# Kernel tuning notes

Measured on AMD Instinct MI355X. Metric: run time of the kernel, lower is better.

## Reference

```python
import jax, jax.numpy as jnp
import numpy as np

# ---- constants hardcoded in the original source ----
N_RBF = 50            # number of RBF policy centers
n = 4                 # cartpole state dim [x, xdot, theta, thetadot]
H = 60                # rollout horizon (hardcoded inside get_future_reward)
DT = 0.05             # dt_outer
KAPPA = 1.0           # UT spread parameter
JITTER = 1e-6
PROC_NOISE = 1e-2     # per-step process noise variance
# dynamics_params = [polemass_length, gravity, length, masspole, total_mass]
PML, G, LEN, MP, MT = 0.05, 9.8, 0.5, 0.1, 1.1

_diag_idx = np.arange(n)
_lr, _lc = np.tril_indices(n, -1)


def _build_L(sp):
    # sp: (N_RBF, n + n(n-1)/2) -> lower-triangular Cholesky factors (N_RBF, n, n)
    L = jnp.zeros((N_RBF, n, n), sp.dtype)
    L = L.at[:, _diag_idx, _diag_idx].set(sp[:, :n])
    L = L.at[:, _lr, _lc].set(sp[:, n:])
    return L


def _policy(params, x):
    # RBF policy: u = sum_i w_i * exp(-(x-mu_i)^T L_i L_i^T (x-mu_i)), clipped to force limits
    w = params[:N_RBF]
    mu = params[N_RBF:N_RBF + n * N_RBF].reshape(n, N_RBF)
    L = _build_L(params[N_RBF + n * N_RBF:].reshape(N_RBF, n + (n * n - n) // 2))
    d = x[:, None] - mu                          # (n, N)
    Ld = jnp.einsum('Nkj,kN->Nj', L, d)          # L_i^T d_i  -> (N, n)
    phi = jnp.exp(-jnp.sum(Ld * Ld, axis=1))     # (N,)
    return jnp.clip(jnp.dot(w, phi), -10.0, 10.0)


def _dyn(x, u):
    # gym cartpole continuous dynamics; x: (4, P) columns of sigma points
    pos, vel, th, thd = x
    s, c = jnp.sin(th), jnp.cos(th)
    temp = (u + PML * thd ** 2 * s) / MT
    thacc = (G * s - c * temp) / (LEN * (4.0 / 3.0 - MP * c * c / MT))
    xacc = temp - PML * thacc * c / MT
    return jnp.stack([vel, xacc, thd, thacc])


def _ut_weights(dtype):
    w0 = KAPPA / (n + KAPPA)
    wi = 1.0 / (2.0 * (n + KAPPA))
    return jnp.concatenate([jnp.array([w0], dtype), jnp.full((2 * n,), wi, dtype)])


def _gen_sigma(mu, cov):
    # standard unscented-transform sigma points from (mu, cov)
    S = jnp.linalg.cholesky(cov + JITTER * jnp.eye(n, dtype=mu.dtype))
    root = jnp.sqrt(n + KAPPA) * S               # (n, n)
    pts = jnp.concatenate([mu[:, None], mu[:, None] + root, mu[:, None] - root], axis=1)  # (n, 2n+1)
    return pts, _ut_weights(mu.dtype)


def _reward(states, weights):
    # quadratic cost UT-mean evaluator
    pos, vel, th, thd = states
    cost = pos ** 2 + vel ** 2 + 10.0 * th ** 2 + thd ** 2
    return -jnp.dot(weights, cost)


def _rollout(params, x0):
    states, weights = _gen_sigma(x0, jnp.zeros((n, n), x0.dtype))  # initialize sigma points at x0

    def body(carry, _):
        states, weights = carry                       # (4, 9), (9,)
        mean = states @ weights                        # UT mean
        u = _policy(params, mean)
        # sigma_point_expand: propagate each point, expand with process-noise UT points
        next_means = states + DT * _dyn(states, u)     # (4, 9)
        cov = PROC_NOISE * DT * jnp.eye(n, dtype=x0.dtype)
        S = jnp.linalg.cholesky(cov + JITTER * jnp.eye(n, dtype=x0.dtype))
        root = jnp.sqrt(n + KAPPA) * S
        offsets = jnp.concatenate([jnp.zeros((n, 1), x0.dtype), root, -root], axis=1)  # (4, 9)
        exp_states = (next_means[:, :, None] + offsets[:, None, :]).reshape(n, -1)      # (4, 81)
        ut_w = _ut_weights(x0.dtype)
        exp_weights = (weights[:, None] * ut_w[None, :]).reshape(-1)                    # (81,)
        # sigma_point_compress: moment-match and regenerate 2n+1 points
        m = exp_states @ exp_weights
        d = exp_states - m[:, None]
        covc = (d * exp_weights) @ d.T
        states, weights = _gen_sigma(m, covc)
        return (states, weights), _reward(states, weights)

    _, rewards = jax.lax.scan(body, (states, weights), None, length=H)
    return jnp.sum(rewards)


def setup_inputs() -> dict:
    key = jax.random.key(0)
    num_params = N_RBF + n * N_RBF + N_RBF * (n + (n * n - n) // 2)  # 750
    param = jax.random.normal(key, (num_params,), jnp.float32) * 0.1
    return {"param": param}


def reference(param):
    x0 = jnp.array([0.0, 0.0, 0.1, 0.0], param.dtype)
    return _rollout(param, x0)
```

## Files before the change

### kernel.cpp

```cpp
#include <hip/hip_runtime.h>
#include <math.h>


template <int CTRL>
__device__ __forceinline__ float dpp_add_f(float v) {
    int s = __builtin_amdgcn_update_dpp(0, __float_as_int(v), CTRL, 0xF, 0xF, true);
    return v + __int_as_float(s);
}
__device__ __forceinline__ float row_sum_f(float v) {
    v = dpp_add_f<0xB1>(v);
    v = dpp_add_f<0x4E>(v);
    v = dpp_add_f<0x124>(v);
    v = dpp_add_f<0x128>(v);
    return v;
}
__device__ __forceinline__ float lane_f(float v, int lane) {
    return __int_as_float(__builtin_amdgcn_readlane(__float_as_int(v), lane));
}
__device__ __forceinline__ float wave_sum_f(float v) {
    v = row_sum_f(v);
    v = dpp_add_f<0x142>(v);
    v = dpp_add_f<0x143>(v);
    return lane_f(v, 63);
}

__global__ __launch_bounds__(64) void horizon_kernel(const float* __restrict__ p,
                                                     float* __restrict__ out) {
    const int l   = threadIdx.x;
    const int l15 = l & 15;
    const int row = l >> 4;

    const float SQL2E = 1.2011224087864498f;

    float w = 0.0f, mu0 = 0.0f, mu1 = 0.0f, mu2 = 0.0f, mu3 = 0.0f;
    float s0=0,s1=0,s2=0,s3=0,s4=0,s5=0,s6=0,s7=0,s8=0,s9=0;
    if (l < 50) {
        w   = p[l];
        mu0 = p[ 50 + l]; mu1 = p[100 + l]; mu2 = p[150 + l]; mu3 = p[200 + l];
        const float* q = p + 250 + 10 * l;
        s0 = q[0]*SQL2E; s1 = q[1]*SQL2E; s2 = q[2]*SQL2E; s3 = q[3]*SQL2E;
        s4 = q[4]*SQL2E; s5 = q[5]*SQL2E; s6 = q[6]*SQL2E; s7 = q[7]*SQL2E;
        s8 = q[8]*SQL2E; s9 = q[9]*SQL2E;
    }

    const float wlf  = (l15 == 0) ? 0.2f : ((l15 < 9) ? 0.1f : 0.0f);
    const float fw5  = 5.0f * wlf;
    const float osgn = (l15 >= 1 && l15 <= 4) ? 1.0f
                     : ((l15 >= 5 && l15 <= 8) ? -1.0f : 0.0f);
    const int   ocol = ((l15 >= 5 ? l15 - 5 : l15 - 1) & 3);

    double mm0 = 0.0, mm1 = 0.0, mm2 = 0.1, mm3 = 0.0;
    float mmf0 = 0.0f, mmf1 = 0.0f, mmf2 = 0.1f, mmf3 = 0.0f;
    float d0 = mmf0 - mu0, d1 = mmf1 - mu1, d2 = mmf2 - mu2, d3 = mmf3 - mu3;
    float frmf = (float)(0.1 * 0.15915494309189535);
    const float CI = 2.2360679774997896e-3f;
    float c00=CI, c10=0.f, c20=0.f, c30=0.f;
    float c11=CI, c21=0.f, c31=0.f;
    float c22=CI, c32=0.f;
    float c33=CI;
    double acc = 0.0;

    const float DIAG5 = 0.00251f;

    #pragma unroll 4
    for (int t = 0; t < 60; ++t) {
        float t0v = fmaf(s0, d0, fmaf(s4, d1, fmaf(s5, d2, s7 * d3)));
        float t1v = fmaf(s1, d1, fmaf(s6, d2, s8 * d3));
        float t2v = fmaf(s2, d2, s9 * d3);
        float t3v = s3 * d3;
        float qn = fmaf(t0v, t0v, fmaf(t1v, t1v, fmaf(t2v, t2v, t3v * t3v)));
        float val = wave_sum_f(w * __builtin_amdgcn_exp2f(-qn));
        float u = fminf(10.0f, fmaxf(-10.0f, val));

        float oo0 = osgn * ((ocol == 0) ? c00 : 0.0f);
        float oo1 = osgn * ((ocol == 0) ? c10 : ((ocol == 1) ? c11 : 0.0f));
        float oo2 = osgn * ((ocol == 0) ? c20 : ((ocol == 1) ? c21 :
                            ((ocol == 2) ? c22 : 0.0f)));
        float oo3 = osgn * ((ocol == 0) ? c30 : ((ocol == 1) ? c31 :
                            ((ocol == 2) ? c32 : c33)));

        float x1 = mmf1 + oo1;
        float x3 = mmf3 + oo3;

        float rv = __builtin_amdgcn_fractf(fmaf(oo2, 0.15915494309189535f, frmf));
        float sn = __builtin_amdgcn_sinf(rv);
        float cs = __builtin_amdgcn_cosf(rv);
        float temp  = fmaf(0.05f * (x3 * x3), sn, u) * 0.9090909090909091f;
        float csc   = cs * cs;
        float den   = fmaf(csc, -0.045454545454545456f, 0.6666666666666666f);
        float rden  = __builtin_amdgcn_rcpf(den);
        float thacc = fmaf(9.8f, sn, -(cs * temp)) * rden;
        float xacc  = fmaf(-0.045454545454545456f, thacc * cs, temp);

        float dl0 = fmaf(0.05f, x1,    oo0);
        float dl1 = fmaf(0.05f, xacc,  oo1);
        float dl2 = fmaf(0.05f, x3,    oo2);
        float dl3 = fmaf(0.05f, thacc, oo3);

        float rd0 = row_sum_f(wlf * dl0);
        float rd1 = row_sum_f(wlf * dl1);
        float rd2 = row_sum_f(wlf * dl2);
        float rd3 = row_sum_f(wlf * dl3);

        mm0 += (double)rd0; mm1 += (double)rd1;
        mm2 += (double)rd2; mm3 += (double)rd3;
        mmf0 = (float)mm0; mmf1 = (float)mm1;
        mmf2 = (float)mm2; mmf3 = (float)mm3;
        d0 = mmf0 - mu0; d1 = mmf1 - mu1; d2 = mmf2 - mu2; d3 = mmf3 - mu3;
        double rev = mm2 * 0.15915494309189535;
        frmf = (float)(rev - floor(rev));

        float v0 = dl0 - rd0, v1 = dl1 - rd1, v2 = dl2 - rd2, v3 = dl3 - rd3;
        float a1 = (row == 0) ? v0 : v3;
        float b1 = (row <= 1) ? v0 : ((row == 2) ? v1 : v3);
        float a2 = (row <= 1) ? v1 : v2;
        float b2 = (row == 0) ? v0 : ((row == 1) ? v1 : v2);
        float a3 = (row <= 1) ? v2 : v3;
        float P1 = row_sum_f(fw5 * a1 * b1);
        float P2 = row_sum_f(fw5 * a2 * b2);
        float P3 = row_sum_f(fw5 * a3 * b2);

        float A00 = lane_f(P1,  0) + DIAG5;
        float A30 = lane_f(P1, 16);
        float A31 = lane_f(P1, 32);
        float A33 = lane_f(P1, 48) + DIAG5;
        float A10 = lane_f(P2,  0);
        float A11 = lane_f(P2, 16) + DIAG5;
        float A22 = lane_f(P2, 32) + DIAG5;
        float A20 = lane_f(P3,  0);
        float A21 = lane_f(P3, 16);
        float A32 = lane_f(P3, 32);

        float rwm = fmaf(mmf0, mmf0, fmaf(mmf1, mmf1,
                    fmaf(10.0f * mmf2, mmf2, mmf3 * mmf3)));
        float rwa = A00 + A11 + 10.0f * A22 + A33;
        acc -= (double)fmaf(0.2f, rwa, rwm);

        float i0 = __builtin_amdgcn_rsqf(A00);
        c00 = A00 * i0;
        c10 = A10 * i0; c20 = A20 * i0; c30 = A30 * i0;
        float b11 = fmaf(-c10, c10, A11);
        float i1 = __builtin_amdgcn_rsqf(b11);
        c11 = b11 * i1;
        c21 = fmaf(-c20, c10, A21) * i1;
        c31 = fmaf(-c30, c10, A31) * i1;
        float b22 = fmaf(-c21, c21, fmaf(-c20, c20, A22));
        float i2 = __builtin_amdgcn_rsqf(b22);
        c22 = b22 * i2;
        c32 = fmaf(-c31, c21, fmaf(-c30, c20, A32)) * i2;
        float b33 = fmaf(-c32, c32, fmaf(-c31, c31, fmaf(-c30, c30, A33)));
        c33 = b33 * __builtin_amdgcn_rsqf(b33);
    }

    if (l == 0) out[0] = (float)acc;
}

extern "C" void kernel_launch(void* const* d_in, const int* in_sizes, int n_in,
                              void* d_out, int out_size, void* d_ws, size_t ws_size,
                              hipStream_t stream) {
    (void)in_sizes; (void)n_in; (void)out_size; (void)d_ws; (void)ws_size;
    const float* p = (const float*)d_in[0];
    float* out = (float*)d_out;
    hipLaunchKernelGGL(horizon_kernel, dim3(1), dim3(64), 0, stream, p, out);
}
```

Baseline: 73.29 us.

## Overlap policy evaluation with covariance update by splitting dynamics affine in control

Rewrites the per-step dynamics so each sigma point's update is affine in the control u (alpha + beta*u). The mean and covariance reductions that do not depend on u can then run before or alongside the RBF policy wave reduction, shortening the serial dependency chain per step. The mean accumulators and the reward accumulator move from double to float, with only the angle phase kept in double. Unroll is lowered from 4 to 2. This adds extra reductions for the beta terms and risks small precision drift from float accumulation.

```diff
diff --git a/kernel.cpp b/kernel.cpp
--- a/kernel.cpp
+++ b/kernel.cpp
@@ -14,23 +14,28 @@
     v = dpp_add_f<0x128>(v);
     return v;
 }
-__device__ __forceinline__ float lane_f(float v, int lane) {
+__device__ __forceinline__ float rl(float v, int lane) {
     return __int_as_float(__builtin_amdgcn_readlane(__float_as_int(v), lane));
 }
 __device__ __forceinline__ float wave_sum_f(float v) {
     v = row_sum_f(v);
     v = dpp_add_f<0x142>(v);
     v = dpp_add_f<0x143>(v);
-    return lane_f(v, 63);
+    return rl(v, 63);
 }
 
 __global__ __launch_bounds__(64) void horizon_kernel(const float* __restrict__ p,
                                                      float* __restrict__ out) {
     const int l   = threadIdx.x;
     const int l15 = l & 15;
-    const int row = l >> 4;
+    const bool r1 = (l >> 4) & 1, r2 = (l >> 4) & 2;
 
-    const float SQL2E = 1.2011224087864498f;
+    const float SQL2E  = 1.2011224087864498f;
+    const float INV_MT = 0.9090909090909091f;
+    const float KCS    = -0.045454545454545456f;
+    const double INV2PI_D = 0.15915494309189535;
+    const float  INV2PI_F = 0.15915494309189535f;
+    const float DIAG5  = 0.00251f;
 
     float w = 0.0f, mu0 = 0.0f, mu1 = 0.0f, mu2 = 0.0f, mu3 = 0.0f;
     float s0=0,s1=0,s2=0,s3=0,s4=0,s5=0,s6=0,s7=0,s8=0,s9=0;
@@ -49,29 +54,19 @@
                      : ((l15 >= 5 && l15 <= 8) ? -1.0f : 0.0f);
     const int   ocol = ((l15 >= 5 ? l15 - 5 : l15 - 1) & 3);
 
-    double mm0 = 0.0, mm1 = 0.0, mm2 = 0.1, mm3 = 0.0;
     float mmf0 = 0.0f, mmf1 = 0.0f, mmf2 = 0.1f, mmf3 = 0.0f;
-    float d0 = mmf0 - mu0, d1 = mmf1 - mu1, d2 = mmf2 - mu2, d3 = mmf3 - mu3;
-    float frmf = (float)(0.1 * 0.15915494309189535);
+    float d0 = -mu0, d1 = -mu1, d2 = 0.1f - mu2, d3 = -mu3;
+    double rev = 0.1 * INV2PI_D;
+    float frmf = (float)rev;
     const float CI = 2.2360679774997896e-3f;
     float c00=CI, c10=0.f, c20=0.f, c30=0.f;
     float c11=CI, c21=0.f, c31=0.f;
     float c22=CI, c32=0.f;
     float c33=CI;
-    double acc = 0.0;
+    float acc = 0.0f;
 
-    const float DIAG5 = 0.00251f;
-
-    #pragma unroll 4
+    #pragma unroll 2
     for (int t = 0; t < 60; ++t) {
-        float t0v = fmaf(s0, d0, fmaf(s4, d1, fmaf(s5, d2, s7 * d3)));
-        float t1v = fmaf(s1, d1, fmaf(s6, d2, s8 * d3));
-        float t2v = fmaf(s2, d2, s9 * d3);
-        float t3v = s3 * d3;
-        float qn = fmaf(t0v, t0v, fmaf(t1v, t1v, fmaf(t2v, t2v, t3v * t3v)));
-        float val = wave_sum_f(w * __builtin_amdgcn_exp2f(-qn));
-        float u = fminf(10.0f, fmaxf(-10.0f, val));
-
         float oo0 = osgn * ((ocol == 0) ? c00 : 0.0f);
         float oo1 = osgn * ((ocol == 0) ? c10 : ((ocol == 1) ? c11 : 0.0f));
         float oo2 = osgn * ((ocol == 0) ? c20 : ((ocol == 1) ? c21 :
@@ -82,77 +77,101 @@
         float x1 = mmf1 + oo1;
         float x3 = mmf3 + oo3;
 
-        float rv = __builtin_amdgcn_fractf(fmaf(oo2, 0.15915494309189535f, frmf));
+        float rv = __builtin_amdgcn_fractf(fmaf(oo2, INV2PI_F, frmf));
         float sn = __builtin_amdgcn_sinf(rv);
         float cs = __builtin_amdgcn_cosf(rv);
-        float temp  = fmaf(0.05f * (x3 * x3), sn, u) * 0.9090909090909091f;
-        float csc   = cs * cs;
-        float den   = fmaf(csc, -0.045454545454545456f, 0.6666666666666666f);
-        float rden  = __builtin_amdgcn_rcpf(den);
-        float thacc = fmaf(9.8f, sn, -(cs * temp)) * rden;
-        float xacc  = fmaf(-0.045454545454545456f, thacc * cs, temp);
+        float a   = (0.045454545454545456f * (x3 * x3)) * sn;
+        float den = fmaf(cs * cs, KCS, 0.6666666666666666f);
+        float rden = __builtin_amdgcn_rcpf(den);
+        float g0 = fmaf(9.8f, sn, -(cs * a)) * rden;
+        float g1 = (-INV_MT) * (cs * rden);
+        float kcs = KCS * cs;
+        float h0 = fmaf(kcs, g0, a);
+        float h1 = fmaf(kcs, g1, INV_MT);
+        float al1 = fmaf(0.05f, h0, oo1), be1 = 0.05f * h1;
+        float al3 = fmaf(0.05f, g0, oo3), be3 = 0.05f * g1;
+        float dl0 = fmaf(0.05f, x1, oo0);
+        float dl2 = fmaf(0.05f, x3, oo2);
 
-        float dl0 = fmaf(0.05f, x1,    oo0);
-        float dl1 = fmaf(0.05f, xacc,  oo1);
-        float dl2 = fmaf(0.05f, x3,    oo2);
-        float dl3 = fmaf(0.05f, thacc, oo3);
+        float selA = r1 ? (r2 ? al3 : al1) : (r2 ? dl2 : dl0);
+        float PA = row_sum_f(wlf * selA);
+        float A0 = rl(PA, 0), A1 = rl(PA, 16), A2 = rl(PA, 32), A3 = rl(PA, 48);
+        float selB = r1 ? (r2 ? be3 : be1) : 0.0f;
+        float PB = row_sum_f(wlf * selB);
+        float B1 = rl(PB, 16), B3 = rl(PB, 48);
 
-        float rd0 = row_sum_f(wlf * dl0);
-        float rd1 = row_sum_f(wlf * dl1);
-        float rd2 = row_sum_f(wlf * dl2);
-        float rd3 = row_sum_f(wlf * dl3);
+        float v0 = dl0 - A0, v2 = dl2 - A2;
+        float va1 = al1 - A1, vb1 = be1 - B1;
+        float va3 = al3 - A3, vb3 = be3 - B3;
+        float sa = r1 ? v2 : v0;
+        sa = r2 ? (r1 ? 0.0f : v2) : sa;
+        float sb = r2 ? v2 : v0;
+        float P1 = row_sum_f((fw5 * sa) * sb);
+        float A00 = rl(P1, 0) + DIAG5, A20 = rl(P1, 16), A22 = rl(P1, 32) + DIAG5;
+        float i0 = __builtin_amdgcn_rsqf(A00);
+        float nc00 = A00 * i0;
+        float nc20 = A20 * i0;
+        float b22p = fmaf(-nc20, nc20, A22);
 
-        mm0 += (double)rd0; mm1 += (double)rd1;
-        mm2 += (double)rd2; mm3 += (double)rd3;
-        mmf0 = (float)mm0; mmf1 = (float)mm1;
-        mmf2 = (float)mm2; mmf3 = (float)mm3;
-        d0 = mmf0 - mu0; d1 = mmf1 - mu1; d2 = mmf2 - mu2; d3 = mmf3 - mu3;
-        double rev = mm2 * 0.15915494309189535;
-        frmf = (float)(rev - floor(rev));
+        float nmm0 = mmf0 + A0, nmm2 = mmf2 + A2;
+        double revn = fma((double)A2, INV2PI_D, rev);
+        rev = revn - floor(revn);
+        float nfrm = (float)rev;
 
-        float v0 = dl0 - rd0, v1 = dl1 - rd1, v2 = dl2 - rd2, v3 = dl3 - rd3;
-        float a1 = (row == 0) ? v0 : v3;
-        float b1 = (row <= 1) ? v0 : ((row == 2) ? v1 : v3);
-        float a2 = (row <= 1) ? v1 : v2;
-        float b2 = (row == 0) ? v0 : ((row == 1) ? v1 : v2);
-        float a3 = (row <= 1) ? v2 : v3;
-        float P1 = row_sum_f(fw5 * a1 * b1);
-        float P2 = row_sum_f(fw5 * a2 * b2);
-        float P3 = row_sum_f(fw5 * a3 * b2);
+        float t0p = fmaf(s0, d0, s5 * d2);
+        float t1p = s6 * d2;
+        float t2p = s2 * d2;
+        float t0v = fmaf(s4, d1, fmaf(s7, d3, t0p));
+        float t1v = fmaf(s1, d1, fmaf(s8, d3, t1p));
+        float t2v = fmaf(s9, d3, t2p);
+        float t3v = s3 * d3;
+        float qn = fmaf(t0v, t0v, fmaf(t1v, t1v, fmaf(t2v, t2v, t3v * t3v)));
+        float val = wave_sum_f(w * __builtin_amdgcn_exp2f(-qn));
+        float u = fminf(10.0f, fmaxf(-10.0f, val));
 
-        float A00 = lane_f(P1,  0) + DIAG5;
-        float A30 = lane_f(P1, 16);
-        float A31 = lane_f(P1, 32);
-        float A33 = lane_f(P1, 48) + DIAG5;
-        float A10 = lane_f(P2,  0);
-        float A11 = lane_f(P2, 16) + DIAG5;
-        float A22 = lane_f(P2, 32) + DIAG5;
-        float A20 = lane_f(P3,  0);
-        float A21 = lane_f(P3, 16);
-        float A32 = lane_f(P3, 32);
+        float rd1 = fmaf(B1, u, A1);
+        float rd3 = fmaf(B3, u, A3);
+        d0 += A0; d2 += A2; d1 += rd1; d3 += rd3;
+        float nmm1 = mmf1 + rd1, nmm3 = mmf3 + rd3;
 
-        float rwm = fmaf(mmf0, mmf0, fmaf(mmf1, mmf1,
-                    fmaf(10.0f * mmf2, mmf2, mmf3 * mmf3)));
+        float v1 = fmaf(vb1, u, va1);
+        float v3 = fmaf(vb3, u, va3);
+        float lo2 = r2 ? v2 : v0, hi2 = r2 ? v3 : v1;
+        float P2 = row_sum_f((fw5 * v1) * (r1 ? hi2 : lo2));
+        float s3a = r1 ? v2 : v0;
+        s3a = r2 ? (r1 ? 0.0f : v3) : s3a;
+        float P3 = row_sum_f((fw5 * v3) * s3a);
+        float A10 = rl(P2, 0), A11 = rl(P2, 16) + DIAG5;
+        float A21 = rl(P2, 32), A31 = rl(P2, 48);
+        float A30 = rl(P3, 0), A32 = rl(P3, 16), A33 = rl(P3, 32) + DIAG5;
+
+        float rwm = fmaf(nmm0, nmm0, fmaf(nmm1, nmm1,
+                    fmaf(10.0f * nmm2, nmm2, nmm3 * nmm3)));
         float rwa = A00 + A11 + 10.0f * A22 + A33;
-        acc -= (double)fmaf(0.2f, rwa, rwm);
+        acc -= fmaf(0.2f, rwa, rwm);
 
-        float i0 = __builtin_amdgcn_rsqf(A00);
-        c00 = A00 * i0;
-        c10 = A10 * i0; c20 = A20 * i0; c30 = A30 * i0;
-        float b11 = fmaf(-c10, c10, A11);
+        float nc10 = A10 * i0;
+        float nc30 = A30 * i0;
+        float b11 = fmaf(-nc10, nc10, A11);
         float i1 = __builtin_amdgcn_rsqf(b11);
-        c11 = b11 * i1;
-        c21 = fmaf(-c20, c10, A21) * i1;
-        c31 = fmaf(-c30, c10, A31) * i1;
-        float b22 = fmaf(-c21, c21, fmaf(-c20, c20, A22));
+        float nc11 = b11 * i1;
+        float nc21 = fmaf(-nc20, nc10, A21) * i1;
+        float nc31 = fmaf(-nc30, nc10, A31) * i1;
+        float b22 = fmaf(-nc21, nc21, b22p);
         float i2 = __builtin_amdgcn_rsqf(b22);
-        c22 = b22 * i2;
-        c32 = fmaf(-c31, c21, fmaf(-c30, c20, A32)) * i2;
-        float b33 = fmaf(-c32, c32, fmaf(-c31, c31, fmaf(-c30, c30, A33)));
-        c33 = b33 * __builtin_amdgcn_rsqf(b33);
+        float nc22 = b22 * i2;
+        float nc32 = fmaf(-nc31, nc21, fmaf(-nc30, nc20, A32)) * i2;
+        float b33 = fmaf(-nc32, nc32, fmaf(-nc31, nc31, fmaf(-nc30, nc30, A33)));
+        float nc33 = b33 * __builtin_amdgcn_rsqf(b33);
+
+        c00 = nc00; c10 = nc10; c20 = nc20; c30 = nc30;
+        c11 = nc11; c21 = nc21; c31 = nc31;
+        c22 = nc22; c32 = nc32; c33 = nc33;
+        mmf0 = nmm0; mmf1 = nmm1; mmf2 = nmm2; mmf3 = nmm3;
+        frmf = nfrm;
     }
 
-    if (l == 0) out[0] = (float)acc;
+    if (l == 0) out[0] = acc;
 }
 
 extern "C" void kernel_launch(void* const* d_in, const int* in_sizes, int n_in,
```

After: 73.15 us. Within noise of the previous version (-0.2%).
